# Performance work log

Hardware: AMD Instinct MI355X
Metric: run time of the kernel (lower is better)

The kernel has to match this reference:

```python
import jax, jax.numpy as jnp
import numpy as np

VOCAB, EMB, HID, TAGS = 50000, 300, 300, 9
B, S = 32, 256


def setup_inputs() -> dict:
    key = jax.random.key(0)
    ks = jax.random.split(key, 16)
    def n(k, shape, s=0.1):
        return jax.random.normal(k, shape, jnp.float32) * s
    return {
        'x': jax.random.randint(ks[0], (B, S), 0, VOCAB),
        'y': jax.random.randint(ks[1], (B, S), 0, TAGS),
        'emb': n(ks[2], (VOCAB, EMB)),
        'w_ih_f': n(ks[3], (4 * HID, EMB)), 'w_hh_f': n(ks[4], (4 * HID, HID)),
        'b_ih_f': n(ks[5], (4 * HID,)), 'b_hh_f': n(ks[6], (4 * HID,)),
        'w_ih_b': n(ks[7], (4 * HID, EMB)), 'w_hh_b': n(ks[8], (4 * HID, HID)),
        'b_ih_b': n(ks[9], (4 * HID,)), 'b_hh_b': n(ks[10], (4 * HID,)),
        'lin_w': n(ks[11], (TAGS, 2 * HID)), 'lin_b': n(ks[12], (TAGS,)),
        'start_t': n(ks[13], (TAGS,)), 'end_t': n(ks[14], (TAGS,)),
        'trans': n(ks[15], (TAGS, TAGS)),
    }


def _lstm_dir(xs, w_ih, w_hh, b_ih, b_hh, reverse):
    # xs: [S, B, E]; PyTorch gate order i, f, g, o
    H = w_hh.shape[1]
    gx = jnp.einsum('sbe,ge->sbg', xs, w_ih) + b_ih  # [S, B, 4H]
    Bsz = xs.shape[1]

    def step(carry, g):
        h, c = carry
        gates = g + h @ w_hh.T + b_hh
        i, f, gg, o = jnp.split(gates, 4, axis=-1)
        c = jax.nn.sigmoid(f) * c + jax.nn.sigmoid(i) * jnp.tanh(gg)
        h = jax.nn.sigmoid(o) * jnp.tanh(c)
        return (h, c), h

    init = (jnp.zeros((Bsz, H), xs.dtype), jnp.zeros((Bsz, H), xs.dtype))
    _, hs = jax.lax.scan(step, init, gx, reverse=reverse)
    return hs  # [S, B, H]


def _forward(x, y, emb, w_ih_f, w_hh_f, b_ih_f, b_hh_f,
             w_ih_b, w_hh_b, b_ih_b, b_hh_b, lin_w, lin_b,
             start_t, end_t, trans):
    e = emb[x]                       # [B, S, E]
    xs = jnp.transpose(e, (1, 0, 2))  # [S, B, E]
    hf = _lstm_dir(xs, w_ih_f, w_hh_f, b_ih_f, b_hh_f, reverse=False)
    hb = _lstm_dir(xs, w_ih_b, w_hh_b, b_ih_b, b_hh_b, reverse=True)
    h = jnp.concatenate([hf, hb], axis=-1)          # [S, B, 2H]
    h = jnp.transpose(h, (1, 0, 2))                  # [B, S, 2H]
    logits = h @ lin_w.T + lin_b                     # [B, S, T]
    probs = jax.nn.softmax(logits, axis=-1)
    emissions = probs                                # (model feeds softmax into CRF, faithful)

    mask = (y != -1)                                 # [B, S] bool
    tags = jnp.where(mask, y, 0)
    mf = mask.astype(emissions.dtype)

    # --- numerator: gold-path score ---
    em_tag = jnp.take_along_axis(emissions, tags[..., None], axis=2)[..., 0]  # [B, S]
    score = start_t[tags[:, 0]] + em_tag[:, 0]
    tp = trans[tags[:, :-1], tags[:, 1:]]            # [B, S-1]
    score = score + jnp.sum((tp + em_tag[:, 1:]) * mf[:, 1:], axis=1)
    last_idx = jnp.sum(mask, axis=1) - 1
    last_tags = jnp.take_along_axis(tags, last_idx[:, None], axis=1)[:, 0]
    score = score + end_t[last_tags]

    # --- denominator: forward algorithm (sequential DP over time) ---
    em_s = jnp.transpose(emissions, (1, 0, 2))       # [S, B, T]
    mask_s = mask.T                                  # [S, B]
    alpha0 = start_t + em_s[0]                       # [B, T]

    def fstep(alpha, inp):
        em_t, m_t = inp
        nxt = jax.nn.logsumexp(alpha[:, :, None] + trans[None], axis=1) + em_t
        return jnp.where(m_t[:, None], nxt, alpha), None

    alpha, _ = jax.lax.scan(fstep, alpha0, (em_s[1:], mask_s[1:]))
    denom = jax.nn.logsumexp(alpha + end_t, axis=1)  # [B]

    llh = jnp.sum(score - denom)                     # torchcrf default reduction='sum'
    loss = -llh                                      # model returns -1 * crf(...)
    return probs, loss


def reference(x, y, emb, w_ih_f, w_hh_f, b_ih_f, b_hh_f,
              w_ih_b, w_hh_b, b_ih_b, b_hh_b, lin_w, lin_b,
              start_t, end_t, trans):
    return _forward(x, y, emb, w_ih_f, w_hh_f, b_ih_f, b_hh_f,
                    w_ih_b, w_hh_b, b_ih_b, b_hh_b, lin_w, lin_b,
                    start_t, end_t, trans)
```

## Files before the change

kernel.cpp:

```cpp
#include <hip/hip_runtime.h>
#include <hip/hip_bf16.h>

typedef __attribute__((ext_vector_type(8))) short s8v;
typedef __attribute__((ext_vector_type(4))) short s4v;
typedef __attribute__((ext_vector_type(4))) float f4v;

#define B_   32
#define S_   256
#define H_   300
#define HP   320
#define NW   19
#define TAGS 9

#define XS_OFF    0
#define HB_OFF    5242880
#define HIST_OFF  5324800
#define EM_OFF    15286272
#define EMTAG_OFF 15581184
#define ARR_OFF   15613952
#define REG_OFF   15616384

#define LOSS_IDX  ((long)B_*S_*TAGS)

__device__ __forceinline__ short f2b(float f) {
  unsigned int u = __builtin_bit_cast(unsigned int, f);
  u = (u + 0x7FFFu + ((u >> 16) & 1u)) >> 16;
  return (short)u;
}
__device__ __forceinline__ float b2f(unsigned int lo16) {
  return __builtin_bit_cast(float, lo16 << 16);
}
__device__ __forceinline__ float sigf(float x) { return 1.f / (1.f + __expf(-x)); }
__device__ __forceinline__ float tanh_f(float x) {
  x = fminf(fmaxf(x, -15.f), 15.f);
  float e = __expf(-2.f * x);
  return (1.f - e) / (1.f + e);
}

__global__ void k_init(const int* __restrict__ x, const float* __restrict__ emb,
                       char* __restrict__ ws) {
  short* xs = (short*)(ws + XS_OFF);
  short* hb = (short*)(ws + HB_OFF);
  int* arr  = (int*)(ws + ARR_OFF);
  long u = (long)blockIdx.x * blockDim.x + threadIdx.x;
  const long N1 = (long)S_ * B_ * 80;
  if (u < N1) {
    int kg = (int)(u % 80);
    long tb = u / 80;
    int b = (int)(tb % B_);
    int t = (int)(tb / B_);
    int k = kg * 4;
    s4v v; v[0]=0; v[1]=0; v[2]=0; v[3]=0;
    if (k + 4 <= H_) {
      int row = x[b * S_ + t];
      f4v q = *(const f4v*)(emb + (long)row * H_ + k);
      v[0]=f2b(q[0]); v[1]=f2b(q[1]); v[2]=f2b(q[2]); v[3]=f2b(q[3]);
    }
    *(s4v*)(xs + ((long)t * B_ + b) * HP + k) = v;
    return;
  }
  u -= N1;
  const long N2 = 2L * 2 * B_ * HP / 4;
  if (u < N2) {
    s4v z; z[0]=0; z[1]=0; z[2]=0; z[3]=0;
    *(s4v*)(hb + u * 4) = z;
    return;
  }
  u -= N2;
  if (u < 704) arr[u] = 0;
}

__launch_bounds__(256, 1)
__global__ void k_lstm(const float* __restrict__ wihf, const float* __restrict__ whhf,
                       const float* __restrict__ bihf, const float* __restrict__ bhhf,
                       const float* __restrict__ wihb, const float* __restrict__ whhb,
                       const float* __restrict__ bihb, const float* __restrict__ bhhb,
                       char* __restrict__ ws) {
  const int slot = blockIdx.x & 7;
  const int idx  = blockIdx.x >> 3;
  if ((slot != 0 && slot != 4) || idx >= NW) return;
  const int dir  = (slot == 4) ? 1 : 0;
  const int wg   = idx;
  const int h0   = wg * 16;
  const int tid  = threadIdx.x;
  const int w    = tid >> 6;
  const int lane = tid & 63;
  const int mhat = w & 1;
  const int khalf= w >> 1;
  const int nl   = lane & 15;
  const int quad = lane >> 4;
  const int hg   = h0 + nl;
  const bool hvalid = hg < H_;

  const float* Wih = dir ? wihb : wihf;
  const float* Whh = dir ? whhb : whhf;
  const float* Bih = dir ? bihb : bihf;
  const float* Bhh = dir ? bhhb : bhhf;

  const short* xs = (const short*)(ws + XS_OFF);
  short* hb = (short*)(ws + HB_OFF);
  unsigned int* hist = (unsigned int*)(ws + HIST_OFF);
  int* arr  = (int*)(ws + ARR_OFF);
  int* ids  = (int*)(ws + REG_OFF);
  int* cnt  = (int*)(ws + REG_OFF + 256);

  __shared__ short sh_xd[2][B_*328];
  __shared__ short sh_h[B_*328];
  __shared__ float red[2*4*64*4];
  __shared__ float shl[B_*17];
  __shared__ int sh_fast;

  unsigned xcd;
  asm volatile("s_getreg_b32 %0, hwreg(HW_REG_XCC_ID)" : "=s"(xcd));
  if (tid == 0) {
    __hip_atomic_store(&ids[dir*NW + wg], (int)(xcd + 1),
                       __ATOMIC_RELAXED, __HIP_MEMORY_SCOPE_AGENT);
    __hip_atomic_fetch_add(&cnt[dir*16], 1, __ATOMIC_ACQ_REL, __HIP_MEMORY_SCOPE_AGENT);
  }

  s8v wf[2][4][5];
  #pragma unroll
  for (int mat = 0; mat < 2; ++mat) {
    const float* W = mat ? Whh : Wih;
    #pragma unroll
    for (int nt = 0; nt < 4; ++nt) {
      const long rowbase = (long)(nt * H_ + hg) * H_;
      #pragma unroll
      for (int kci = 0; kci < 5; ++kci) {
        int kb = (khalf*5 + kci)*32 + quad*8;
        s8v v; v[0]=0;v[1]=0;v[2]=0;v[3]=0;v[4]=0;v[5]=0;v[6]=0;v[7]=0;
        if (hvalid) {
          #pragma unroll
          for (int half = 0; half < 2; ++half) {
            int k0 = kb + half*4;
            if (k0 + 4 <= H_) {
              f4v q = *(const f4v*)(W + rowbase + k0);
              v[half*4+0] = f2b(q[0]);
              v[half*4+1] = f2b(q[1]);
              v[half*4+2] = f2b(q[2]);
              v[half*4+3] = f2b(q[3]);
            } else {
              #pragma unroll
              for (int j = 0; j < 4; ++j) {
                int k = k0 + j;
                if (k < H_) v[half*4+j] = f2b(W[rowbase + k]);
              }
            }
          }
        }
        wf[mat][nt][kci] = v;
      }
    }
  }

  float bias[4];
  #pragma unroll
  for (int nt = 0; nt < 4; ++nt)
    bias[nt] = hvalid ? (Bih[nt*H_ + hg] + Bhh[nt*H_ + hg]) : 0.f;

  if (tid == 0) {
    while (__hip_atomic_load(&cnt[dir*16], __ATOMIC_ACQUIRE, __HIP_MEMORY_SCOPE_AGENT) < NW) {}
    int ok = 1; const int mine = (int)(xcd + 1);
    for (int i = 0; i < NW; ++i)
      ok &= (__hip_atomic_load(&ids[dir*NW + i], __ATOMIC_RELAXED,
                               __HIP_MEMORY_SCOPE_AGENT) == mine);
    sh_fast = ok;
  }

  float creg[4] = {0.f, 0.f, 0.f, 0.f};
  const int arow = (mhat*16 + nl) * 328 + quad * 8;

  int soff[5], loff[5];
  #pragma unroll
  for (int i = 0; i < 5; ++i) {
    int u = tid + i*256;
    int b = u / 40, kg = u % 40;
    soff[i] = b*HP  + kg*8;
    loff[i] = b*328 + kg*8;
  }

  {
    const int t0 = dir ? (S_ - 1) : 0;
    const short* xsrc = xs + (long)t0 * B_ * HP;
    #pragma unroll
    for (int i = 0; i < 5; ++i)
      *(s8v*)&sh_xd[0][loff[i]] = *(const s8v*)&xsrc[soff[i]];
  }
  __syncthreads();
  const bool FAST = (sh_fast != 0);

  for (int s = 0; s < S_; ++s) {
    const int t = dir ? (S_ - 1 - s) : s;
    const short* xcur = &sh_xd[s & 1][0];

    f4v acc[4];
    #pragma unroll
    for (int nt = 0; nt < 4; ++nt) { acc[nt][0]=0.f; acc[nt][1]=0.f; acc[nt][2]=0.f; acc[nt][3]=0.f; }

    #pragma unroll
    for (int kci = 0; kci < 5; ++kci) {
      s8v a = *(const s8v*)&xcur[arow + (khalf*5 + kci)*32];
      #pragma unroll
      for (int nt = 0; nt < 4; ++nt)
        acc[nt] = __builtin_amdgcn_mfma_f32_16x16x32_bf16(a, wf[0][nt][kci], acc[nt], 0, 0, 0);
    }

    s8v xl[5];
    if (s + 1 < S_) {
      const int tn = dir ? (S_ - 2 - s) : (s + 1);
      const short* xsrc = xs + (long)tn * B_ * HP;
      #pragma unroll
      for (int i = 0; i < 5; ++i)
        xl[i] = *(const s8v*)&xsrc[soff[i]];
    }

    if (s > 0 && tid < NW) {
      if (FAST) {
        unsigned long long fl = (unsigned long long)&arr[(dir*NW + tid)*16];
        unsigned v;
        do {
          asm volatile("global_atomic_or %0, %1, %2, off sc0\n\ts_waitcnt vmcnt(0)"
                       : "=&v"(v) : "v"(fl), "v"(0u) : "memory");
        } while ((int)v < s);
      } else {
        const int* fl = &arr[(dir*NW + tid)*16];
        while (__hip_atomic_load(fl, __ATOMIC_ACQUIRE, __HIP_MEMORY_SCOPE_AGENT) < s) { }
      }
    }
    __syncthreads();

    {
      const short* hsrc = hb + (long)(dir*2 + (s & 1)) * B_ * HP;
      if (FAST) {
        s8v r0, r1, r2, r3, r4;
        const void* p0 = &hsrc[soff[0]];
        const void* p1 = &hsrc[soff[1]];
        const void* p2 = &hsrc[soff[2]];
        const void* p3 = &hsrc[soff[3]];
        const void* p4 = &hsrc[soff[4]];
        asm volatile(
          "global_load_dwordx4 %0, %5, off sc0\n\t"
          "global_load_dwordx4 %1, %6, off sc0\n\t"
          "global_load_dwordx4 %2, %7, off sc0\n\t"
          "global_load_dwordx4 %3, %8, off sc0\n\t"
          "global_load_dwordx4 %4, %9, off sc0\n\t"
          "s_waitcnt vmcnt(0)"
          : "=&v"(r0), "=&v"(r1), "=&v"(r2), "=&v"(r3), "=&v"(r4)
          : "v"(p0), "v"(p1), "v"(p2), "v"(p3), "v"(p4)
          : "memory");
        *(s8v*)&sh_h[loff[0]] = r0;
        *(s8v*)&sh_h[loff[1]] = r1;
        *(s8v*)&sh_h[loff[2]] = r2;
        *(s8v*)&sh_h[loff[3]] = r3;
        *(s8v*)&sh_h[loff[4]] = r4;
      } else {
        #pragma unroll
        for (int i = 0; i < 5; ++i)
          *(s8v*)&sh_h[loff[i]] = *(const s8v*)&hsrc[soff[i]];
      }
    }
    __syncthreads();

    #pragma unroll
    for (int kci = 0; kci < 5; ++kci) {
      s8v a = *(const s8v*)&sh_h[arow + (khalf*5 + kci)*32];
      #pragma unroll
      for (int nt = 0; nt < 4; ++nt)
        acc[nt] = __builtin_amdgcn_mfma_f32_16x16x32_bf16(a, wf[1][nt][kci], acc[nt], 0, 0, 0);
    }

    if (khalf == 1) {
      #pragma unroll
      for (int nt = 0; nt < 4; ++nt)
        *(f4v*)&red[((mhat*4 + nt)*64 + lane)*4] = acc[nt];
    }
    __syncthreads();

    if (khalf == 0) {
      #pragma unroll
      for (int nt = 0; nt < 4; ++nt) {
        f4v o = *(const f4v*)&red[((mhat*4 + nt)*64 + lane)*4];
        acc[nt][0]+=o[0]; acc[nt][1]+=o[1]; acc[nt][2]+=o[2]; acc[nt][3]+=o[3];
      }
      #pragma unroll
      for (int r = 0; r < 4; ++r) {
        int b = mhat*16 + quad*4 + r;
        float gi = acc[0][r] + bias[0];
        float gf = acc[1][r] + bias[1];
        float gg = acc[2][r] + bias[2];
        float go = acc[3][r] + bias[3];
        float c  = sigf(gf) * creg[r] + sigf(gi) * tanh_f(gg);
        float h  = sigf(go) * tanh_f(c);
        creg[r] = c;
        shl[b*17 + nl] = h;
      }
    }
    if (s + 1 < S_) {
      short* xnxt = &sh_xd[(s + 1) & 1][0];
      #pragma unroll
      for (int i = 0; i < 5; ++i)
        *(s8v*)&xnxt[loff[i]] = xl[i];
    }
    __syncthreads();

    {
      int b = tid >> 3, j = tid & 7;
      float fa = shl[b*17 + 2*j];
      float fb = shl[b*17 + 2*j + 1];
      unsigned int pack = (unsigned int)(unsigned short)f2b(fa) |
                          ((unsigned int)(unsigned short)f2b(fb) << 16);
      unsigned int* dsti = (unsigned int*)(hb + (long)(dir*2 + ((s+1) & 1)) * B_ * HP);
      if (FAST) {
        dsti[b*160 + (h0 >> 1) + j] = pack;
      } else {
        __hip_atomic_store(&dsti[b*160 + (h0 >> 1) + j], pack,
                           __ATOMIC_RELAXED, __HIP_MEMORY_SCOPE_AGENT);
      }
      hist[((long)t * B_ + b) * 304 + dir*152 + (h0 >> 1) + j] = pack;
    }
    __syncthreads();
    if (s + 1 < S_ && tid == 0) {
      if (FAST) {
        unsigned long long fl = (unsigned long long)&arr[(dir*NW + wg)*16];
        asm volatile("global_atomic_swap %0, %1, off"
                     :: "v"(fl), "v"((unsigned)(s + 1)) : "memory");
      } else {
        __hip_atomic_store(&arr[(dir*NW + wg)*16], s + 1,
                           __ATOMIC_RELEASE, __HIP_MEMORY_SCOPE_AGENT);
      }
    }
  }
}

__global__ void k_logits(const int* __restrict__ y,
                         const float* __restrict__ lin_w, const float* __restrict__ lin_b,
                         char* __restrict__ ws, float* __restrict__ out) {
  __shared__ float lw[600*10];
  const unsigned int* hist = (const unsigned int*)(ws + HIST_OFF);
  float* em    = (float*)(ws + EM_OFF);
  float* emtag = (float*)(ws + EMTAG_OFF);
  int tid = threadIdx.x;
  for (int i = tid; i < 600*TAGS; i += 256) {
    int j = i / TAGS, tg = i % TAGS;
    lw[j*10 + tg] = lin_w[tg*600 + j];
  }
  __syncthreads();

  int g = blockIdx.x * 256 + tid;
  int b = g & 31, t = g >> 5;
  const unsigned int* hrow = hist + ((long)t * B_ + b) * 304;

  float lg[TAGS];
  #pragma unroll
  for (int tg = 0; tg < TAGS; ++tg) lg[tg] = lin_b[tg];

  for (int jd = 0; jd < 150; ++jd) {
    unsigned int v = hrow[jd];
    float ha = b2f(v & 0xffffu), hc = b2f(v >> 16);
    int j0 = 2*jd;
    #pragma unroll
    for (int tg = 0; tg < TAGS; ++tg)
      lg[tg] += ha * lw[j0*10 + tg] + hc * lw[(j0+1)*10 + tg];
  }
  for (int jd = 0; jd < 150; ++jd) {
    unsigned int v = hrow[152 + jd];
    float ha = b2f(v & 0xffffu), hc = b2f(v >> 16);
    int j0 = 300 + 2*jd;
    #pragma unroll
    for (int tg = 0; tg < TAGS; ++tg)
      lg[tg] += ha * lw[j0*10 + tg] + hc * lw[(j0+1)*10 + tg];
  }

  float m = lg[0];
  #pragma unroll
  for (int tg = 1; tg < TAGS; ++tg) m = fmaxf(m, lg[tg]);
  float p[TAGS]; float sum = 0.f;
  #pragma unroll
  for (int tg = 0; tg < TAGS; ++tg) { p[tg] = __expf(lg[tg] - m); sum += p[tg]; }
  float inv = 1.f / sum;

  int yy = y[b*S_ + t];
  int sel = (yy != -1) ? yy : 0;
  float et = 0.f;
  #pragma unroll
  for (int tg = 0; tg < TAGS; ++tg) {
    float pv = p[tg] * inv;
    out[((long)b*S_ + t)*TAGS + tg] = pv;
    em[((long)t*B_ + b)*TAGS + tg] = pv;
    if (tg == sel) et = pv;
  }
  emtag[t*B_ + b] = et;
}

__global__ void k_crf(const int* __restrict__ y,
                      const float* __restrict__ start_t, const float* __restrict__ end_t,
                      const float* __restrict__ trans,
                      char* __restrict__ ws, float* __restrict__ out) {
  __shared__ float tr[81], st[TAGS], en[TAGS];
  __shared__ float alpha[2][B_][12];
  __shared__ float resS[B_], resD[B_];
  const float* em    = (const float*)(ws + EM_OFF);
  const float* emtag = (const float*)(ws + EMTAG_OFF);
  int tid = threadIdx.x;
  if (tid < 81) tr[tid] = trans[tid];
  if (tid < TAGS) { st[tid] = start_t[tid]; en[tid] = end_t[tid]; }
  __syncthreads();

  for (int it = tid; it < B_*TAGS; it += 256) {
    int b = it / TAGS, j = it % TAGS;
    alpha[0][b][j] = st[j] + em[(0*B_ + b)*TAGS + j];
  }

  if (tid < B_) {
    int b = tid;
    int y0 = y[b*S_]; bool m0 = (y0 != -1); int tg0 = m0 ? y0 : 0;
    float score = st[tg0] + emtag[0*B_ + b];
    int cnt = m0 ? 1 : 0;
    int prev = tg0;
    for (int t = 1; t < S_; ++t) {
      int yt = y[b*S_ + t]; bool mt = (yt != -1); int tg = mt ? yt : 0;
      float mf = mt ? 1.f : 0.f;
      score += (tr[prev*TAGS + tg] + emtag[t*B_ + b]) * mf;
      prev = tg;
      cnt += mt ? 1 : 0;
    }
    int li = cnt - 1; if (li < 0) li = 0;
    int yl = y[b*S_ + li]; int tgl = (yl != -1) ? yl : 0;
    score += en[tgl];
    resS[b] = score;
  }
  __syncthreads();

  for (int t = 1; t < S_; ++t) {
    int pb = (t-1) & 1, cb2 = t & 1;
    for (int it = tid; it < B_*TAGS; it += 256) {
      int b = it / TAGS, j = it % TAGS;
      float a[TAGS]; float m = -1e30f;
      #pragma unroll
      for (int i = 0; i < TAGS; ++i) { a[i] = alpha[pb][b][i] + tr[i*TAGS + j]; m = fmaxf(m, a[i]); }
      float ssum = 0.f;
      #pragma unroll
      for (int i = 0; i < TAGS; ++i) ssum += __expf(a[i] - m);
      float v = m + __logf(ssum) + em[((long)t*B_ + b)*TAGS + j];
      bool mt = (y[b*S_ + t] != -1);
      alpha[cb2][b][j] = mt ? v : alpha[pb][b][j];
    }
    __syncthreads();
  }

  int fb = (S_-1) & 1;
  if (tid < B_) {
    int b = tid;
    float a[TAGS]; float m = -1e30f;
    #pragma unroll
    for (int i = 0; i < TAGS; ++i) { a[i] = alpha[fb][b][i] + en[i]; m = fmaxf(m, a[i]); }
    float ssum = 0.f;
    #pragma unroll
    for (int i = 0; i < TAGS; ++i) ssum += __expf(a[i] - m);
    resD[b] = m + __logf(ssum);
  }
  __syncthreads();
  if (tid == 0) {
    float llh = 0.f;
    for (int bb = 0; bb < B_; ++bb) llh += resS[bb] - resD[bb];
    out[LOSS_IDX] = -llh;
  }
}

extern "C" void kernel_launch(void* const* d_in, const int* in_sizes, int n_in,
                              void* d_out, int out_size, void* d_ws, size_t ws_size,
                              hipStream_t stream) {
  const int* x = (const int*)d_in[0];
  const int* y = (const int*)d_in[1];
  const float* emb   = (const float*)d_in[2];
  const float* wihf  = (const float*)d_in[3];
  const float* whhf  = (const float*)d_in[4];
  const float* bihf  = (const float*)d_in[5];
  const float* bhhf  = (const float*)d_in[6];
  const float* wihb  = (const float*)d_in[7];
  const float* whhb  = (const float*)d_in[8];
  const float* bihb  = (const float*)d_in[9];
  const float* bhhb  = (const float*)d_in[10];
  const float* lin_w = (const float*)d_in[11];
  const float* lin_b = (const float*)d_in[12];
  const float* sta   = (const float*)d_in[13];
  const float* endt  = (const float*)d_in[14];
  const float* trans = (const float*)d_in[15];
  char* ws = (char*)d_ws;
  float* out = (float*)d_out;

  const long n_init = (long)S_*B_*80 + 2L*2*B_*HP/4 + 704;
  int grid_init = (int)((n_init + 255) / 256);
  k_init<<<grid_init, 256, 0, stream>>>(x, emb, ws);
  k_lstm<<<152, 256, 0, stream>>>(wihf, whhf, bihf, bhhf,
                                  wihb, whhb, bihb, bhhb, ws);
  k_logits<<<(B_*S_)/256, 256, 0, stream>>>(y, lin_w, lin_b, ws, out);
  k_crf<<<1, 256, 0, stream>>>(y, sta, endt, trans, ws, out);
}
```

Measured before the change: 1.072 ms.

## Stage CRF inputs in LDS with emission prefetch; defer history store past flag

The CRF kernel now copies the tag labels (as bytes) and the per-position gold emissions into shared memory up front. Each timestep's emission row is prefetched into a double-buffered shared ring one step ahead, so the sequential forward recursion stops issuing dependent global loads. In the LSTM recurrence kernel, the store to the hidden-state history buffer is moved after the cross-workgroup progress flag is published, taking it off the critical path of the inter-workgroup handoff. The cost is extra shared memory in the CRF kernel and an upfront load phase.

```diff
diff --git a/kernel.cpp b/kernel.cpp
--- a/kernel.cpp
+++ b/kernel.cpp
@@ -303,20 +303,20 @@
     }
     __syncthreads();
 
+    const int pb_ = tid >> 3, pj = tid & 7;
+    unsigned int pack;
     {
-      int b = tid >> 3, j = tid & 7;
-      float fa = shl[b*17 + 2*j];
-      float fb = shl[b*17 + 2*j + 1];
-      unsigned int pack = (unsigned int)(unsigned short)f2b(fa) |
-                          ((unsigned int)(unsigned short)f2b(fb) << 16);
+      float fa = shl[pb_*17 + 2*pj];
+      float fb = shl[pb_*17 + 2*pj + 1];
+      pack = (unsigned int)(unsigned short)f2b(fa) |
+             ((unsigned int)(unsigned short)f2b(fb) << 16);
       unsigned int* dsti = (unsigned int*)(hb + (long)(dir*2 + ((s+1) & 1)) * B_ * HP);
       if (FAST) {
-        dsti[b*160 + (h0 >> 1) + j] = pack;
+        dsti[pb_*160 + (h0 >> 1) + pj] = pack;
       } else {
-        __hip_atomic_store(&dsti[b*160 + (h0 >> 1) + j], pack,
+        __hip_atomic_store(&dsti[pb_*160 + (h0 >> 1) + pj], pack,
                            __ATOMIC_RELAXED, __HIP_MEMORY_SCOPE_AGENT);
       }
-      hist[((long)t * B_ + b) * 304 + dir*152 + (h0 >> 1) + j] = pack;
     }
     __syncthreads();
     if (s + 1 < S_ && tid == 0) {
@@ -329,6 +329,7 @@
                            __ATOMIC_RELEASE, __HIP_MEMORY_SCOPE_AGENT);
       }
     }
+    hist[((long)t * B_ + pb_) * 304 + dir*152 + (h0 >> 1) + pj] = pack;
   }
 }
 
@@ -397,35 +398,42 @@
                       const float* __restrict__ trans,
                       char* __restrict__ ws, float* __restrict__ out) {
   __shared__ float tr[81], st[TAGS], en[TAGS];
+  __shared__ signed char yc[B_*S_];
+  __shared__ float emt[S_*B_];
+  __shared__ float ring[2][B_*TAGS];
   __shared__ float alpha[2][B_][12];
   __shared__ float resS[B_], resD[B_];
   const float* em    = (const float*)(ws + EM_OFF);
   const float* emtag = (const float*)(ws + EMTAG_OFF);
-  int tid = threadIdx.x;
+  const int tid = threadIdx.x;
   if (tid < 81) tr[tid] = trans[tid];
   if (tid < TAGS) { st[tid] = start_t[tid]; en[tid] = end_t[tid]; }
+  for (int i = tid; i < B_*S_; i += 256) yc[i] = (signed char)y[i];
+  for (int i = tid; i < S_*B_; i += 256) emt[i] = emtag[i];
+  for (int i = tid; i < 2*B_*TAGS; i += 256) ((float*)ring)[i] = em[i];
   __syncthreads();
 
   for (int it = tid; it < B_*TAGS; it += 256) {
     int b = it / TAGS, j = it % TAGS;
-    alpha[0][b][j] = st[j] + em[(0*B_ + b)*TAGS + j];
+    alpha[0][b][j] = st[j] + ring[0][b*TAGS + j];
   }
 
   if (tid < B_) {
-    int b = tid;
-    int y0 = y[b*S_]; bool m0 = (y0 != -1); int tg0 = m0 ? y0 : 0;
-    float score = st[tg0] + emtag[0*B_ + b];
+    const int b = tid;
+    const signed char* yr = &yc[b*S_];
+    int y0 = yr[0]; bool m0 = (y0 != -1); int tg0 = m0 ? y0 : 0;
+    float score = st[tg0] + emt[0*B_ + b];
     int cnt = m0 ? 1 : 0;
     int prev = tg0;
     for (int t = 1; t < S_; ++t) {
-      int yt = y[b*S_ + t]; bool mt = (yt != -1); int tg = mt ? yt : 0;
+      int yt = yr[t]; bool mt = (yt != -1); int tg = mt ? yt : 0;
       float mf = mt ? 1.f : 0.f;
-      score += (tr[prev*TAGS + tg] + emtag[t*B_ + b]) * mf;
+      score += (tr[prev*TAGS + tg] + emt[t*B_ + b]) * mf;
       prev = tg;
       cnt += mt ? 1 : 0;
     }
     int li = cnt - 1; if (li < 0) li = 0;
-    int yl = y[b*S_ + li]; int tgl = (yl != -1) ? yl : 0;
+    int yl = yr[li]; int tgl = (yl != -1) ? yl : 0;
     score += en[tgl];
     resS[b] = score;
   }
@@ -433,6 +441,10 @@
 
   for (int t = 1; t < S_; ++t) {
     int pb = (t-1) & 1, cb2 = t & 1;
+    if (t + 1 < S_) {
+      for (int i = tid; i < B_*TAGS; i += 256)
+        ring[(t+1) & 1][i] = em[(long)(t+1)*B_*TAGS + i];
+    }
     for (int it = tid; it < B_*TAGS; it += 256) {
       int b = it / TAGS, j = it % TAGS;
       float a[TAGS]; float m = -1e30f;
@@ -441,16 +453,16 @@
       float ssum = 0.f;
       #pragma unroll
       for (int i = 0; i < TAGS; ++i) ssum += __expf(a[i] - m);
-      float v = m + __logf(ssum) + em[((long)t*B_ + b)*TAGS + j];
-      bool mt = (y[b*S_ + t] != -1);
+      float v = m + __logf(ssum) + ring[t & 1][b*TAGS + j];
+      bool mt = (yc[b*S_ + t] != -1);
       alpha[cb2][b][j] = mt ? v : alpha[pb][b][j];
     }
     __syncthreads();
   }
 
-  int fb = (S_-1) & 1;
+  const int fb = (S_-1) & 1;
   if (tid < B_) {
-    int b = tid;
+    const int b = tid;
     float a[TAGS]; float m = -1e30f;
     #pragma unroll
     for (int i = 0; i < TAGS; ++i) { a[i] = alpha[fb][b][i] + en[i]; m = fmaxf(m, a[i]); }
```

After: 1.169 ms. +9.1%, slower.
